# Kernel tuning notes

Measured on AMD Instinct MI355X. Metric: run time of the kernel, lower is better.

Reference implementation:

```python
import jax, jax.numpy as jnp
import numpy as np

N = 8192
F_IN = 128
D = 128
NEG_SLOPE = 0.2  # cfg.negativeslope (standard GAT value)
MASK_FILL = -9e15


def setup_inputs() -> dict:
    key = jax.random.key(0)
    k1, k2, k3, k4 = jax.random.split(key, 4)
    A = jax.random.randint(k1, (N, N), 0, 2, dtype=jnp.int32)
    X = jax.random.normal(k2, (N, F_IN), dtype=jnp.float32)
    # glorot init for Ws, xavier_uniform(gain=1.414) for a
    lim_w = float(np.sqrt(6.0 / (F_IN + D)))
    Ws = jax.random.uniform(k3, (F_IN, D), minval=-lim_w, maxval=lim_w, dtype=jnp.float32)
    lim_a = 1.414 * float(np.sqrt(6.0 / (2 * D + 1)))
    a = jax.random.uniform(k4, (2 * D, 1), minval=-lim_a, maxval=lim_a, dtype=jnp.float32)
    return {"A": A, "X": X, "Ws": Ws, "a": a}


def reference(A, X, Ws, a):
    # Wh: [N, D]
    Wh = X @ Ws
    d = Wh.shape[-1]
    # additive attention: e_ij = leaky_relu(Wh_i . a1 + Wh_j . a2)
    e1 = Wh @ a[:d]          # [N, 1]
    e2 = Wh @ a[d:]          # [N, 1]
    e = jax.nn.leaky_relu(e1 + e2.T, negative_slope=NEG_SLOPE)  # [N, N]
    e = jnp.where(A > 0, e, MASK_FILL)
    attn = jax.nn.softmax(e, axis=1)  # row-wise over neighbors
    H = attn @ Wh            # [N, D]
    return H
```

## Files before the change

### kernel.cpp

```cpp
#include <hip/hip_runtime.h>
#include <hip/hip_bf16.h>

#define NN 8192
#define DD 128

typedef __attribute__((ext_vector_type(8))) short short8;
typedef __attribute__((ext_vector_type(4))) float f32x4;
typedef __attribute__((ext_vector_type(4))) int i32x4;
typedef unsigned int u32;

__device__ __forceinline__ ushort f2bf(float f) {
    __hip_bfloat16 h = __float2bfloat16(f);
    return *(ushort*)&h;
}

__device__ __forceinline__ void async_ld16(const void* g, void* l) {
    __builtin_amdgcn_global_load_lds(
        (const __attribute__((address_space(1))) u32*)g,
        (__attribute__((address_space(3))) u32*)l, 16, 0, 0);
}

__global__ __launch_bounds__(256) void k12_gemm(const float* __restrict__ X,
                                                const float* __restrict__ Ws,
                                                const float* __restrict__ a,
                                                ushort* __restrict__ WhT,
                                                float* __restrict__ C1,
                                                float* __restrict__ C1s,
                                                float2* __restrict__ E2) {
    __shared__ float lWs[128 * 132];
    __shared__ float lX[32 * 132];
    __shared__ ushort lT2[128 * 32];
    __shared__ float la[256];
    int t = threadIdx.x, bx = blockIdx.x;
    la[t] = a[t];
    const float4* Ws4 = (const float4*)Ws;
    const float4* X4 = (const float4*)X;
    for (int j = 0; j < 16; ++j) {
        int u = j * 256 + t;
        int k = u >> 5, c4 = u & 31;
        *(float4*)&lWs[k * 132 + c4 * 4] = Ws4[u];
    }
    for (int j = 0; j < 4; ++j) {
        int u = j * 256 + t;
        int r = u >> 5, c4 = u & 31;
        *(float4*)&lX[r * 132 + c4 * 4] = X4[bx * 1024 + u];
    }
    __syncthreads();
    int r0 = (t >> 5) * 4, c0 = (t & 31) * 4;
    float acc[4][4];
#pragma unroll
    for (int i = 0; i < 4; ++i)
#pragma unroll
        for (int j = 0; j < 4; ++j) acc[i][j] = 0.f;
#pragma unroll 4
    for (int k = 0; k < 128; ++k) {
        float4 wv = *(const float4*)&lWs[k * 132 + c0];
        float x0 = lX[(r0 + 0) * 132 + k];
        float x1 = lX[(r0 + 1) * 132 + k];
        float x2 = lX[(r0 + 2) * 132 + k];
        float x3 = lX[(r0 + 3) * 132 + k];
#pragma unroll
        for (int j = 0; j < 4; ++j) {
            acc[0][j] += x0 * ((const float*)&wv)[j];
            acc[1][j] += x1 * ((const float*)&wv)[j];
            acc[2][j] += x2 * ((const float*)&wv)[j];
            acc[3][j] += x3 * ((const float*)&wv)[j];
        }
    }
#pragma unroll
    for (int i = 0; i < 4; ++i)
#pragma unroll
        for (int j = 0; j < 4; ++j)
            lT2[(c0 + j) * 32 + r0 + i] = f2bf(acc[i][j]);
    float p1[4], p2[4];
#pragma unroll
    for (int i = 0; i < 4; ++i) {
        p1[i] = 0.f; p2[i] = 0.f;
#pragma unroll
        for (int j = 0; j < 4; ++j) {
            p1[i] += acc[i][j] * la[c0 + j];
            p2[i] += acc[i][j] * la[128 + c0 + j];
        }
    }
#pragma unroll
    for (int m = 1; m < 32; m <<= 1) {
#pragma unroll
        for (int i = 0; i < 4; ++i) {
            p1[i] += __shfl_xor(p1[i], m);
            p2[i] += __shfl_xor(p2[i], m);
        }
    }
    if ((t & 31) == 0) {
#pragma unroll
        for (int i = 0; i < 4; ++i) {
            int row = bx * 32 + r0 + i;
            C1[row]  = __expf(p1[i]);
            C1s[row] = __expf(0.2f * p1[i]);
            E2[row]  = make_float2(__expf(p2[i]), __expf(0.2f * p2[i]));
        }
    }
    __syncthreads();
    {
        int d = t >> 1, hf = t & 1;
        uint4* dst = (uint4*)&WhT[(size_t)d * NN + bx * 32 + hf * 16];
        const uint4* src = (const uint4*)&lT2[d * 32 + hf * 16];
        dst[0] = src[0];
        dst[1] = src[1];
    }
}

#define PACK4(b, v, sh)                                     \
    b |= (u32)((v).x & 1) << (sh);                          \
    b |= (u32)((v).y & 1) << ((sh) + 1);                    \
    b |= (u32)((v).z & 1) << ((sh) + 2);                    \
    b |= (u32)((v).w & 1) << ((sh) + 3);

__global__ __launch_bounds__(256, 3) void k3_main(
    const int* __restrict__ A, const ushort* __restrict__ WhT,
    const float* __restrict__ C1, const float* __restrict__ C1s,
    const float2* __restrict__ E2,
    float* __restrict__ Hp, float* __restrict__ Lp) {

    __shared__ __align__(16) char lB[2 * 16384];
    __shared__ __align__(16) char lE[2 * 1024];

    int tid = threadIdx.x;
    int lane = tid & 63;
    int w = tid >> 6;
    int n = lane & 15;
    int kg = lane >> 4;

    int bx = blockIdx.x;
    int kb = blockIdx.y;
    int rb = bx * 128 + w * 32;

    float c1_0 = C1[rb + n],      c1s_0 = C1s[rb + n];
    float c1_1 = C1[rb + 16 + n], c1s_1 = C1s[rb + 16 + n];

    const char* srcB[4];
    char* dstB[4];
#pragma unroll
    for (int i = 0; i < 4; ++i) {
        int p = 4 * w + i;
        int c = p & 7, tp = p >> 3;
        srcB[i] = (const char*)(WhT + (size_t)(c * 16 + n) * NN +
                                (size_t)kb * 512 + tp * 32 + kg * 8);
        dstB[i] = lB + p * 1024 + lane * 16;
    }
    const char* srcE = (const char*)(E2 + (size_t)kb * 512) + lane * 16;

    const int* pA0 = A + (size_t)(rb + n) * NN + (size_t)kb * 512 + kg * 8;
    const int* pA1 = pA0 + (size_t)16 * NN;

    i32x4 ar[8];
    u32 a_cur0, a_cur1;

#pragma unroll
    for (int tp = 0; tp < 2; ++tp) {
        ar[tp * 2 + 0]     = __builtin_nontemporal_load((const i32x4*)(pA0 + tp * 32));
        ar[tp * 2 + 1]     = __builtin_nontemporal_load((const i32x4*)(pA0 + tp * 32 + 4));
        ar[4 + tp * 2 + 0] = __builtin_nontemporal_load((const i32x4*)(pA1 + tp * 32));
        ar[4 + tp * 2 + 1] = __builtin_nontemporal_load((const i32x4*)(pA1 + tp * 32 + 4));
    }
#pragma unroll
    for (int i = 0; i < 4; ++i) async_ld16(srcB[i], dstB[i]);
    if (w == 0) async_ld16(srcE, lE + lane * 16);
    {
        u32 b0 = 0, b1 = 0;
#pragma unroll
        for (int tp = 0; tp < 2; ++tp) {
            PACK4(b0, ar[tp * 2 + 0], tp * 8);
            PACK4(b0, ar[tp * 2 + 1], tp * 8 + 4);
            PACK4(b1, ar[4 + tp * 2 + 0], tp * 8);
            PACK4(b1, ar[4 + tp * 2 + 1], tp * 8 + 4);
        }
        a_cur0 = b0; a_cur1 = b1;
    }

    short8 ones;
#pragma unroll
    for (int j = 0; j < 8; ++j) ones[j] = (short)0x3F80;

    f32x4 acc0[8], acc1[8];
#pragma unroll
    for (int c = 0; c < 8; ++c) {
        acc0[c] = (f32x4){0.f, 0.f, 0.f, 0.f};
        acc1[c] = (f32x4){0.f, 0.f, 0.f, 0.f};
    }
    f32x4 accl0 = (f32x4){0.f, 0.f, 0.f, 0.f};
    f32x4 accl1 = (f32x4){0.f, 0.f, 0.f, 0.f};

    __syncthreads();

    for (int kt = 0; kt < 8; ++kt) {
        int buf = kt & 1;
        if (kt < 7) {
#pragma unroll
            for (int tp = 0; tp < 2; ++tp) {
                ar[tp * 2 + 0]     = __builtin_nontemporal_load((const i32x4*)(pA0 + (kt + 1) * 64 + tp * 32));
                ar[tp * 2 + 1]     = __builtin_nontemporal_load((const i32x4*)(pA0 + (kt + 1) * 64 + tp * 32 + 4));
                ar[4 + tp * 2 + 0] = __builtin_nontemporal_load((const i32x4*)(pA1 + (kt + 1) * 64 + tp * 32));
                ar[4 + tp * 2 + 1] = __builtin_nontemporal_load((const i32x4*)(pA1 + (kt + 1) * 64 + tp * 32 + 4));
            }
            int bo = (buf ^ 1) * 16384;
#pragma unroll
            for (int i = 0; i < 4; ++i)
                async_ld16(srcB[i] + (kt + 1) * 128, dstB[i] + bo);
        }
        if (w == 1 && (kt & 1) == 0 && kt < 6)
            async_ld16(srcE + (kt / 2 + 1) * 1024,
                       lE + (((kt >> 1) + 1) & 1) * 1024 + lane * 16);

        const char* bB = lB + buf * 16384;
        const float* bE = (const float*)(lE + ((kt >> 1) & 1) * 1024) + (kt & 1) * 128;
#pragma unroll
        for (int tp = 0; tp < 2; ++tp) {
            const float4* ev = (const float4*)(bE + (tp * 32 + kg * 8) * 2);
            float pe[16];
            *(float4*)(pe + 0)  = ev[0];
            *(float4*)(pe + 4)  = ev[1];
            *(float4*)(pe + 8)  = ev[2];
            *(float4*)(pe + 12) = ev[3];
            u32 ab0 = (a_cur0 >> (tp * 8)) & 0xffu;
            u32 ab1 = (a_cur1 >> (tp * 8)) & 0xffu;
            short8 af0, af1;
#pragma unroll
            for (int u = 0; u < 8; ++u) {
                float w0 = fmaxf(c1_0 * pe[2 * u], c1s_0 * pe[2 * u + 1]);
                float w1 = fmaxf(c1_1 * pe[2 * u], c1s_1 * pe[2 * u + 1]);
                af0[u] = ((ab0 >> u) & 1u) ? (short)f2bf(w0) : (short)0;
                af1[u] = ((ab1 >> u) & 1u) ? (short)f2bf(w1) : (short)0;
            }
            const short8* bb = (const short8*)(bB + tp * 8192);
#pragma unroll
            for (int c = 0; c < 8; ++c) {
                short8 bf = bb[c * 64 + lane];
                acc0[c] = __builtin_amdgcn_mfma_f32_16x16x32_bf16(af0, bf, acc0[c], 0, 0, 0);
                acc1[c] = __builtin_amdgcn_mfma_f32_16x16x32_bf16(af1, bf, acc1[c], 0, 0, 0);
            }
            accl0 = __builtin_amdgcn_mfma_f32_16x16x32_bf16(af0, ones, accl0, 0, 0, 0);
            accl1 = __builtin_amdgcn_mfma_f32_16x16x32_bf16(af1, ones, accl1, 0, 0, 0);
        }
        if (kt < 7) {
            u32 b0 = 0, b1 = 0;
#pragma unroll
            for (int tp = 0; tp < 2; ++tp) {
                PACK4(b0, ar[tp * 2 + 0], tp * 8);
                PACK4(b0, ar[tp * 2 + 1], tp * 8 + 4);
                PACK4(b1, ar[4 + tp * 2 + 0], tp * 8);
                PACK4(b1, ar[4 + tp * 2 + 1], tp * 8 + 4);
            }
            a_cur0 = b0; a_cur1 = b1;
        }
        __syncthreads();
    }

    float* Hpb = Hp + (size_t)kb * (NN * DD);
#pragma unroll
    for (int c = 0; c < 8; ++c)
#pragma unroll
        for (int r = 0; r < 4; ++r) {
            Hpb[(size_t)(rb + kg * 4 + r) * DD + c * 16 + n]      = acc0[c][r];
            Hpb[(size_t)(rb + 16 + kg * 4 + r) * DD + c * 16 + n] = acc1[c][r];
        }
    if (n == 0) {
        float* Lpb = Lp + (size_t)kb * NN;
#pragma unroll
        for (int r = 0; r < 4; ++r) {
            Lpb[rb + kg * 4 + r]      = accl0[r];
            Lpb[rb + 16 + kg * 4 + r] = accl1[r];
        }
    }
}

__global__ void k4_final(const float* __restrict__ Hp, const float* __restrict__ Lp,
                         float* __restrict__ out) {
    int g = blockIdx.x * 256 + threadIdx.x;
    int i = g >> 5;
    float4 sv = make_float4(0.f, 0.f, 0.f, 0.f);
    float l = 0.f;
#pragma unroll
    for (int kb = 0; kb < 16; ++kb) {
        float4 v = *(const float4*)(Hp + (size_t)kb * (NN * DD) + (size_t)g * 4);
        sv.x += v.x; sv.y += v.y; sv.z += v.z; sv.w += v.w;
        l += Lp[(size_t)kb * NN + i];
    }
    float r = 1.f / l;
    *(float4*)(out + (size_t)g * 4) = make_float4(sv.x * r, sv.y * r, sv.z * r, sv.w * r);
}

extern "C" void kernel_launch(void* const* d_in, const int* in_sizes, int n_in,
                              void* d_out, int out_size, void* d_ws, size_t ws_size,
                              hipStream_t stream) {
    const int*   A  = (const int*)d_in[0];
    const float* X  = (const float*)d_in[1];
    const float* Ws = (const float*)d_in[2];
    const float* a  = (const float*)d_in[3];
    float* out = (float*)d_out;

    char* ws = (char*)d_ws;
    ushort* WhT = (ushort*)(ws);
    float*  C1  = (float*)(ws + (2u << 20));
    float*  C1s = (float*)(ws + (2u << 20) + (32u << 10));
    float2* E2  = (float2*)(ws + (2u << 20) + (64u << 10));
    float*  Hp  = (float*)(ws + (3u << 20));
    float*  Lp  = (float*)(ws + (67u << 20));

    k12_gemm<<<256, 256, 0, stream>>>(X, Ws, a, WhT, C1, C1s, E2);
    k3_main<<<dim3(64, 16), 256, 0, stream>>>(A, WhT, C1, C1s, E2, Hp, Lp);
    k4_final<<<1024, 256, 0, stream>>>(Hp, Lp, out);
}
```

Before: 407.8 us.

## Preload whole WhT K-slab into LDS with 512-thread blocks, drop per-step syncs

The main kernel now uses 512-thread blocks that each cover 256 rows, and loads the entire 512-column slab of WhT (128 KB) and E2 into LDS once at the start. The double-buffered per-iteration async loads and the per-iteration barriers are gone. This doubles reuse of each B tile across rows and removes barrier stalls inside the loop. The cost is far higher LDS use per block, which limits occupancy to about one block per CU, and an up-front load with no overlap against compute.

```diff
diff --git a/kernel.cpp b/kernel.cpp
--- a/kernel.cpp
+++ b/kernel.cpp
@@ -115,14 +115,14 @@
     b |= (u32)((v).z & 1) << ((sh) + 2);                    \
     b |= (u32)((v).w & 1) << ((sh) + 3);
 
-__global__ __launch_bounds__(256, 3) void k3_main(
+__global__ __launch_bounds__(512, 2) void k3_main(
     const int* __restrict__ A, const ushort* __restrict__ WhT,
     const float* __restrict__ C1, const float* __restrict__ C1s,
     const float2* __restrict__ E2,
     float* __restrict__ Hp, float* __restrict__ Lp) {
 
-    __shared__ __align__(16) char lB[2 * 16384];
-    __shared__ __align__(16) char lE[2 * 1024];
+    __shared__ __align__(16) char lB[131072];
+    __shared__ __align__(16) char lE[4096];
 
     int tid = threadIdx.x;
     int lane = tid & 63;
@@ -132,22 +132,10 @@
 
     int bx = blockIdx.x;
     int kb = blockIdx.y;
-    int rb = bx * 128 + w * 32;
+    int rb = bx * 256 + w * 32;
 
     float c1_0 = C1[rb + n],      c1s_0 = C1s[rb + n];
     float c1_1 = C1[rb + 16 + n], c1s_1 = C1s[rb + 16 + n];
-
-    const char* srcB[4];
-    char* dstB[4];
-#pragma unroll
-    for (int i = 0; i < 4; ++i) {
-        int p = 4 * w + i;
-        int c = p & 7, tp = p >> 3;
-        srcB[i] = (const char*)(WhT + (size_t)(c * 16 + n) * NN +
-                                (size_t)kb * 512 + tp * 32 + kg * 8);
-        dstB[i] = lB + p * 1024 + lane * 16;
-    }
-    const char* srcE = (const char*)(E2 + (size_t)kb * 512) + lane * 16;
 
     const int* pA0 = A + (size_t)(rb + n) * NN + (size_t)kb * 512 + kg * 8;
     const int* pA1 = pA0 + (size_t)16 * NN;
@@ -162,9 +150,21 @@
         ar[4 + tp * 2 + 0] = __builtin_nontemporal_load((const i32x4*)(pA1 + tp * 32));
         ar[4 + tp * 2 + 1] = __builtin_nontemporal_load((const i32x4*)(pA1 + tp * 32 + 4));
     }
-#pragma unroll
-    for (int i = 0; i < 4; ++i) async_ld16(srcB[i], dstB[i]);
-    if (w == 0) async_ld16(srcE, lE + lane * 16);
+
+#pragma unroll
+    for (int i = 0; i < 16; ++i) {
+        int p = w + i * 8;
+        int kt = p >> 4, tp = (p >> 3) & 1, c = p & 7;
+        const ushort* src = WhT + (size_t)(c * 16 + n) * NN +
+                            (size_t)kb * 512 + kt * 64 + tp * 32 + kg * 8;
+        async_ld16(src, lB + p * 1024 + lane * 16);
+    }
+    if (w == 0)
+#pragma unroll
+        for (int i = 0; i < 4; ++i)
+            async_ld16((const char*)(E2 + (size_t)kb * 512) + (i * 64 + lane) * 16,
+                       lE + (i * 64 + lane) * 16);
+
     {
         u32 b0 = 0, b1 = 0;
 #pragma unroll
@@ -193,7 +193,6 @@
     __syncthreads();
 
     for (int kt = 0; kt < 8; ++kt) {
-        int buf = kt & 1;
         if (kt < 7) {
 #pragma unroll
             for (int tp = 0; tp < 2; ++tp) {
@@ -202,20 +201,11 @@
                 ar[4 + tp * 2 + 0] = __builtin_nontemporal_load((const i32x4*)(pA1 + (kt + 1) * 64 + tp * 32));
                 ar[4 + tp * 2 + 1] = __builtin_nontemporal_load((const i32x4*)(pA1 + (kt + 1) * 64 + tp * 32 + 4));
             }
-            int bo = (buf ^ 1) * 16384;
-#pragma unroll
-            for (int i = 0; i < 4; ++i)
-                async_ld16(srcB[i] + (kt + 1) * 128, dstB[i] + bo);
-        }
-        if (w == 1 && (kt & 1) == 0 && kt < 6)
-            async_ld16(srcE + (kt / 2 + 1) * 1024,
-                       lE + (((kt >> 1) + 1) & 1) * 1024 + lane * 16);
-
-        const char* bB = lB + buf * 16384;
-        const float* bE = (const float*)(lE + ((kt >> 1) & 1) * 1024) + (kt & 1) * 128;
+        }
 #pragma unroll
         for (int tp = 0; tp < 2; ++tp) {
-            const float4* ev = (const float4*)(bE + (tp * 32 + kg * 8) * 2);
+            const float4* ev = (const float4*)((const float*)lE +
+                                               (kt * 64 + tp * 32 + kg * 8) * 2);
             float pe[16];
             *(float4*)(pe + 0)  = ev[0];
             *(float4*)(pe + 4)  = ev[1];
@@ -231,7 +221,7 @@
                 af0[u] = ((ab0 >> u) & 1u) ? (short)f2bf(w0) : (short)0;
                 af1[u] = ((ab1 >> u) & 1u) ? (short)f2bf(w1) : (short)0;
             }
-            const short8* bb = (const short8*)(bB + tp * 8192);
+            const short8* bb = (const short8*)(lB + (kt * 16 + tp * 8) * 1024);
 #pragma unroll
             for (int c = 0; c < 8; ++c) {
                 short8 bf = bb[c * 64 + lane];
@@ -252,7 +242,6 @@
             }
             a_cur0 = b0; a_cur1 = b1;
         }
-        __syncthreads();
     }
 
     float* Hpb = Hp + (size_t)kb * (NN * DD);
@@ -307,6 +296,6 @@
     float*  Lp  = (float*)(ws + (67u << 20));
 
     k12_gemm<<<256, 256, 0, stream>>>(X, Ws, a, WhT, C1, C1s, E2);
-    k3_main<<<dim3(64, 16), 256, 0, stream>>>(A, WhT, C1, C1s, E2, Hp, Lp);
+    k3_main<<<dim3(32, 16), 512, 0, stream>>>(A, WhT, C1, C1s, E2, Hp, Lp);
     k4_final<<<1024, 256, 0, stream>>>(Hp, Lp, out);
 }
```

Result: no change. 412.1 us (+1.1%).
